# Performance work log

Hardware: AMD Instinct MI355X
Metric: run time of the kernel (lower is better)

## Reference

```python
import jax, jax.numpy as jnp
import numpy as np

B, S, D, HID, NH, R = 64, 2048, 512, 512, 8, 4
DH = D // NH
EPS = 1e-4


def setup_inputs() -> dict:
    key = jax.random.key(0)
    ks = jax.random.split(key, 32)
    w = lambda k, shape: 0.02 * jax.random.normal(k, shape, dtype=jnp.float32)
    embeddings = jax.random.normal(ks[0], (B, S, D), dtype=jnp.float32)
    attention_mask = jax.random.randint(ks[1], (B, S), 0, 2).astype(jnp.int32)
    attention_mask = attention_mask.at[:, 0].set(1)  # guarantee >=1 valid token
    return {
        'embeddings': embeddings,
        'attention_mask': attention_mask,
        # Theory-of-Mind pooled attention
        'Wk': w(ks[2], (D, D)), 'Wv': w(ks[3], (D, D)),
        'q_tom': w(ks[4], (NH, DH)), 'W_tom_fuse': w(ks[5], (D, D)),
        'w_hp': w(ks[6], (D, 1)), 'b_hp': jnp.zeros((1,), jnp.float32),
        # GCACU
        'Wg1': w(ks[7], (D, HID)), 'bg1': jnp.zeros((HID,), jnp.float32),
        'Wg2': w(ks[8], (HID, D)), 'bg2': jnp.zeros((D,), jnp.float32),
        'w_inc': w(ks[9], (D, 1)), 'b_inc': jnp.zeros((1,), jnp.float32),
        # CLoST head (setup/punchline means -> humor prob)
        'Wc1': w(ks[10], (2 * D, HID)), 'bc1': jnp.zeros((HID,), jnp.float32),
        'wc2': w(ks[11], (HID, 1)), 'bc2': jnp.zeros((1,), jnp.float32),
        # mHC low-rank stream mixing
        'U_mhc': w(ks[12], (3, R)), 'V_mhc': w(ks[13], (R, 3)),
        # SEVADE evaluator
        'Ws1': w(ks[14], (D + 3, HID)), 'bs1': jnp.zeros((HID,), jnp.float32),
        'ws2': w(ks[15], (HID, 1)), 'bs2': jnp.zeros((1,), jnp.float32),
        # final head
        'Wf1': w(ks[16], (D + 3, HID)), 'bf1': jnp.zeros((HID,), jnp.float32),
        'wf2': w(ks[17], (HID, 1)), 'bf2': jnp.zeros((1,), jnp.float32),
    }


def safe_logit(p, eps=EPS):
    p = jnp.clip(p, eps, 1.0 - eps)
    return jnp.log(p / (1.0 - p))


def _forward(embeddings, attention_mask, Wk, Wv, q_tom, W_tom_fuse, w_hp, b_hp,
             Wg1, bg1, Wg2, bg2, w_inc, b_inc, Wc1, bc1, wc2, bc2,
             U_mhc, V_mhc, Ws1, bs1, ws2, bs2, Wf1, bf1, wf2, bf2):
    x = embeddings  # [B,S,D]
    m = attention_mask.astype(x.dtype)  # [B,S]

    # --- ToM: learned-query pooled multi-head attention ---
    k = (x @ Wk).reshape(x.shape[0], x.shape[1], NH, DH)  # [B,S,H,dh]
    v = (x @ Wv).reshape(x.shape[0], x.shape[1], NH, DH)
    scores = jnp.einsum('hd,bshd->bhs', q_tom, k) / jnp.sqrt(jnp.float32(DH))
    scores = jnp.where(m[:, None, :] > 0, scores, -1e9)
    attn = jax.nn.softmax(scores, axis=-1)  # [B,H,S]
    fused = jnp.einsum('bhs,bshd->bhd', attn, v).reshape(x.shape[0], D)
    fused_mental = fused @ W_tom_fuse  # [B,D]
    tom_hp = jax.nn.sigmoid(fused_mental @ w_hp + b_hp)  # [B,1]

    # --- GCACU: masked mean -> MLP contextual stream + incongruity ---
    denom = jnp.sum(m, axis=1, keepdims=True)  # [B,1]
    mean_tok = jnp.sum(x * m[..., None], axis=1) / denom  # [B,D]
    ctx = jax.nn.relu(mean_tok @ Wg1 + bg1) @ Wg2 + bg2  # [B,D]
    inc = jax.nn.sigmoid(ctx @ w_inc + b_inc)  # [B,1]

    # --- CLoST: vectorized ragged setup/punchline split (torch code loops per sample) ---
    cum = jnp.cumsum(m, axis=1)  # rank of each valid token, [B,S]
    valid_count = cum[:, -1]  # [B]
    split = jnp.maximum(1, jnp.floor(valid_count * 0.6).astype(jnp.int32)).astype(x.dtype)
    setup_mask = m * (cum <= split[:, None])
    punch_mask = m * (cum > split[:, None])
    punch_cnt = jnp.sum(punch_mask, axis=1, keepdims=True)
    last_mask = m * (cum == valid_count[:, None])  # fallback: last valid token
    punch_mask = jnp.where(punch_cnt > 0, punch_mask, last_mask)
    setup_mean = jnp.sum(x * setup_mask[..., None], 1) / jnp.sum(setup_mask, 1)[:, None]
    punch_mean = jnp.sum(x * punch_mask[..., None], 1) / jnp.sum(punch_mask, 1)[:, None]
    h = jax.nn.relu(jnp.concatenate([setup_mean, punch_mean], -1) @ Wc1 + bc1)
    clost_prob = jax.nn.sigmoid(h @ wc2 + bc2)  # [B,1]
    clost_stream = 0.5 * (setup_mean + punch_mean)  # [B,D]

    scores3 = jnp.concatenate([tom_hp, inc, clost_prob], axis=1)  # [B,3]
    streams = jnp.stack([fused_mental, ctx, clost_stream], axis=1)  # [B,3,D]

    # --- mHC: residual low-rank stream mixing + manifold (unit-norm) constraint ---
    M = jnp.eye(3, dtype=x.dtype) + U_mhc @ V_mhc  # [3,3]
    mixed = jnp.einsum('st,btd->bsd', M, streams)
    mixed = mixed / (jnp.linalg.norm(mixed, axis=-1, keepdims=True) + 1e-6)

    # --- SEVADE evaluator ---
    sev_in = jnp.concatenate([mixed.mean(axis=1), scores3], axis=-1)
    sev_logits = jax.nn.relu(sev_in @ Ws1 + bs1) @ ws2 + bs2  # [B,1]

    # --- final head + logit fusion ---
    pooled = mixed.mean(axis=1)  # [B,D]
    fused_logits = jax.nn.relu(jnp.concatenate([pooled, scores3], -1) @ Wf1 + bf1) @ wf2 + bf2
    logits = fused_logits + 0.5 * sev_logits + 0.1 * safe_logit(scores3.mean(axis=1, keepdims=True))
    return logits  # [B,1]


def reference(embeddings, attention_mask, Wk, Wv, q_tom, W_tom_fuse, w_hp, b_hp,
              Wg1, bg1, Wg2, bg2, w_inc, b_inc, Wc1, bc1, wc2, bc2,
              U_mhc, V_mhc, Ws1, bs1, ws2, bs2, Wf1, bf1, wf2, bf2):
    return _forward(embeddings, attention_mask, Wk, Wv, q_tom, W_tom_fuse, w_hp, b_hp,
                    Wg1, bg1, Wg2, bg2, w_inc, b_inc, Wc1, bc1, wc2, bc2,
                    U_mhc, V_mhc, Ws1, bs1, ws2, bs2, Wf1, bf1, wf2, bf2)
```

## Files before the change

### kernel.cpp

```cpp
#include <hip/hip_runtime.h>
#include <math.h>

#define B_  64
#define S_  2048
#define D_  512
#define NH_ 8

static const size_t OFF_WKEFF  = 0;
static const size_t OFF_SSUM   = 4096;
static const size_t OFF_PSUM   = OFF_SSUM   + 32768;
static const size_t OFF_LSUM   = OFF_PSUM   + 32768;
static const size_t OFF_XAPART = OFF_LSUM   + 512;
static const size_t OFF_XA     = OFF_XAPART + 4194304;
static const size_t OFF_FUSED  = OFF_XA     + 262144;
static const size_t OFF_FM     = OFF_FUSED  + 32768;
static const size_t OFF_MEANT  = OFF_FM     + 32768;
static const size_t OFF_CATSP  = OFF_MEANT  + 32768;
static const size_t OFF_CLOST  = OFF_CATSP  + 65536;
static const size_t OFF_G1     = OFF_CLOST  + 32768;
static const size_t OFF_CTX    = OFF_G1     + 32768;
static const size_t OFF_HC     = OFF_CTX    + 32768;
static const size_t OFF_S3     = OFF_HC     + 32768;
static const size_t OFF_HEADIN = OFF_S3     + 256;
static const size_t OFF_HS     = OFF_HEADIN + 33280;
static const size_t OFF_HF     = OFF_HS     + 32768;
static const size_t OFF_MINFO  = OFF_HF     + 32768;

__global__ __launch_bounds__(256) void k_prep(const float* __restrict__ Wk,
                                              const float* __restrict__ q,
                                              const int* __restrict__ mask,
                                              float* __restrict__ zbase,
                                              float* __restrict__ wkeff,
                                              int* __restrict__ minfo) {
    int bx = blockIdx.x, tid = threadIdx.x;
    if (bx < 258) {
        int i = bx * 256 + tid;
        if (i < 66048) zbase[i] = 0.f;
        return;
    }
    if (bx < 274) {
        int idx = (bx - 258) * 256 + tid;
        int h = idx >> 9, e = idx & 511;
        float s = 0.f;
        #pragma unroll 8
        for (int d = 0; d < 64; ++d) s = fmaf(Wk[e * 512 + h * 64 + d], q[h * 64 + d], s);
        wkeff[h * 512 + e] = s * 0.125f;
        return;
    }
    {
        int b = bx - 274;
        __shared__ int sh[256];
        int m8[8]; int cnt = 0; int s0 = tid * 8;
        #pragma unroll
        for (int i = 0; i < 8; ++i) { m8[i] = mask[b * S_ + s0 + i] > 0; cnt += m8[i]; }
        sh[tid] = cnt; __syncthreads();
        for (int off = 1; off < 256; off <<= 1) {
            int add = (tid >= off) ? sh[tid - off] : 0;
            __syncthreads();
            sh[tid] += add;
            __syncthreads();
        }
        int total  = sh[255];
        int before = sh[tid] - cnt;
        int split  = max(1, (int)floorf((float)total * 0.6f));
        int cum = before;
        #pragma unroll
        for (int i = 0; i < 8; ++i) {
            if (m8[i]) {
                cum++;
                if (cum == split) minfo[b * 8 + 2] = s0 + i;
                if (cum == total) minfo[b * 8 + 3] = s0 + i;
            }
        }
        if (tid == 0) { minfo[b * 8 + 0] = total; minfo[b * 8 + 1] = split; }
    }
}

__global__ __launch_bounds__(256, 4) void k_main(const float* __restrict__ x,
                                                 const int* __restrict__ mask,
                                                 const float* __restrict__ wkeff,
                                                 const int* __restrict__ minfo,
                                                 float* __restrict__ ssum,
                                                 float* __restrict__ psum,
                                                 float* __restrict__ lsum,
                                                 float* __restrict__ xapart) {
    const int b = blockIdx.x, chunk = blockIdx.y;
    const int tid = threadIdx.x, hg = tid >> 6, lane = tid & 63;
    const int h0 = hg * 2;
    const int col0 = lane * 8;

    float wk0[8], wk1[8];
    #pragma unroll
    for (int i = 0; i < 8; ++i) {
        wk0[i] = wkeff[h0 * 512 + col0 + i];
        wk1[i] = wkeff[(h0 + 1) * 512 + col0 + i];
    }

    const int boundary = minfo[b * 8 + 2];
    const float* xb = x + (size_t)b * (S_ * D_);
    const int* mb = mask + b * S_;
    const int sb = chunk * 128;

    int m0 = mb[sb + lane];
    int m1 = mb[sb + 64 + lane];

    float xacc0[8], xacc1[8], sacc[8], pacc[8];
    #pragma unroll
    for (int i = 0; i < 8; ++i) { xacc0[i] = 0.f; xacc1[i] = 0.f; sacc[i] = 0.f; pacc[i] = 0.f; }
    float lacc0 = 0.f, lacc1 = 0.f;

    const float* base = xb + (size_t)sb * D_ + col0;
    float4 A0 = *(const float4*)(base);
    float4 A1 = *(const float4*)(base + 4);
    float4 B0 = *(const float4*)(base + D_);
    float4 B1 = *(const float4*)(base + D_ + 4);

    for (int t = 0; t < 128; t += 2) {
        float xa8[8] = {A0.x, A0.y, A0.z, A0.w, A1.x, A1.y, A1.z, A1.w};
        float xb8[8] = {B0.x, B0.y, B0.z, B0.w, B1.x, B1.y, B1.z, B1.w};
        if (t + 2 < 128) {
            const float* nb = base + (size_t)(t + 2) * D_;
            A0 = *(const float4*)(nb);
            A1 = *(const float4*)(nb + 4);
            B0 = *(const float4*)(nb + D_);
            B1 = *(const float4*)(nb + D_ + 4);
        }
        float s00 = xa8[0] * wk0[0], s01 = xa8[0] * wk1[0];
        float s10 = xb8[0] * wk0[0], s11 = xb8[0] * wk1[0];
        #pragma unroll
        for (int i = 1; i < 8; ++i) {
            s00 = fmaf(xa8[i], wk0[i], s00);
            s01 = fmaf(xa8[i], wk1[i], s01);
            s10 = fmaf(xb8[i], wk0[i], s10);
            s11 = fmaf(xb8[i], wk1[i], s11);
        }
        #pragma unroll
        for (int d = 1; d < 64; d <<= 1) {
            s00 += __shfl_xor(s00, d, 64);
            s01 += __shfl_xor(s01, d, 64);
            s10 += __shfl_xor(s10, d, 64);
            s11 += __shfl_xor(s11, d, 64);
        }
        int mreg = (t & 64) ? m1 : m0;
        int mm0 = __shfl(mreg, t & 63, 64);
        int mm1 = __shfl(mreg, (t + 1) & 63, 64);
        int sg0 = sb + t, sg1 = sb + t + 1;

        float w00 = (mm0 > 0) ? __expf(s00) : 0.f;
        float w01 = (mm0 > 0) ? __expf(s01) : 0.f;
        float w10 = (mm1 > 0) ? __expf(s10) : 0.f;
        float w11 = (mm1 > 0) ? __expf(s11) : 0.f;
        lacc0 += w00 + w10;
        lacc1 += w01 + w11;
        #pragma unroll
        for (int i = 0; i < 8; ++i) {
            xacc0[i] = fmaf(w10, xb8[i], fmaf(w00, xa8[i], xacc0[i]));
            xacc1[i] = fmaf(w11, xb8[i], fmaf(w01, xa8[i], xacc1[i]));
        }
        if (hg == 0) {
            float fs0 = (mm0 > 0 && sg0 <= boundary) ? 1.f : 0.f;
            float fp0 = (mm0 > 0 && sg0 >  boundary) ? 1.f : 0.f;
            float fs1 = (mm1 > 0 && sg1 <= boundary) ? 1.f : 0.f;
            float fp1 = (mm1 > 0 && sg1 >  boundary) ? 1.f : 0.f;
            #pragma unroll
            for (int i = 0; i < 8; ++i) {
                sacc[i] = fmaf(fs1, xb8[i], fmaf(fs0, xa8[i], sacc[i]));
                pacc[i] = fmaf(fp1, xb8[i], fmaf(fp0, xa8[i], pacc[i]));
            }
        }
    }

    float* d0 = xapart + (((size_t)b * 16 + chunk) * 8 + h0) * 512 + col0;
    float* d1 = d0 + 512;
    ((float4*)d0)[0] = make_float4(xacc0[0], xacc0[1], xacc0[2], xacc0[3]);
    ((float4*)d0)[1] = make_float4(xacc0[4], xacc0[5], xacc0[6], xacc0[7]);
    ((float4*)d1)[0] = make_float4(xacc1[0], xacc1[1], xacc1[2], xacc1[3]);
    ((float4*)d1)[1] = make_float4(xacc1[4], xacc1[5], xacc1[6], xacc1[7]);
    if (lane == 0) {
        atomicAdd(&lsum[b * 8 + h0],     lacc0);
        atomicAdd(&lsum[b * 8 + h0 + 1], lacc1);
    }
    if (hg == 0) {
        #pragma unroll
        for (int i = 0; i < 8; ++i) {
            atomicAdd(&ssum[b * 512 + col0 + i], sacc[i]);
            atomicAdd(&psum[b * 512 + col0 + i], pacc[i]);
        }
    }
}

__global__ __launch_bounds__(256) void k_xared(const float* __restrict__ part,
                                               const float* __restrict__ lsum,
                                               float* __restrict__ xa) {
    int idx = blockIdx.x * 256 + threadIdx.x;
    int b = idx >> 12, j = idx & 4095, h = j >> 9;
    float s = 0.f;
    #pragma unroll
    for (int c = 0; c < 16; ++c) s += part[((size_t)(b * 16 + c)) * 4096 + j];
    xa[idx] = s / lsum[b * 8 + h];
}

__global__ __launch_bounds__(256) void k_means(const float* __restrict__ x,
                                               const float* __restrict__ ssum,
                                               const float* __restrict__ psum,
                                               const int* __restrict__ minfo,
                                               float* __restrict__ meantok,
                                               float* __restrict__ catsp,
                                               float* __restrict__ clost) {
    int b = blockIdx.x;
    int e = blockIdx.y * 256 + threadIdx.x;
    int total = minfo[b * 8 + 0], split = minfo[b * 8 + 1], last = minfo[b * 8 + 3];
    int pcnt = total - split;
    float ssv = ssum[b * 512 + e], psv = psum[b * 512 + e];
    float mt = (ssv + psv) / (float)total;
    float sm = ssv / (float)split;
    float pm = (pcnt > 0) ? psv / (float)pcnt : x[((size_t)b * S_ + last) * D_ + e];
    meantok[b * 512 + e] = mt;
    catsp[b * 1024 + e] = sm;
    catsp[b * 1024 + 512 + e] = pm;
    clost[b * 512 + e] = 0.5f * (sm + pm);
}

__global__ __launch_bounds__(256) void k_gemv3(
    const float* A0_, int lda0, const float* W0_, const float* bi0_, float* o0_, int K0, int r0, int hm0,
    const float* A1_, int lda1, const float* W1_, const float* bi1_, float* o1_, int K1, int r1, int hm1,
    const float* A2_, int lda2, const float* W2_, const float* bi2_, float* o2_, int K2, int r2, int hm2) {
    const float* A; const float* W; const float* bias; float* out;
    int lda, K, relu_, hm;
    int z = blockIdx.z;
    if (z == 0)      { A = A0_; lda = lda0; W = W0_; bias = bi0_; out = o0_; K = K0; relu_ = r0; hm = hm0; }
    else if (z == 1) { A = A1_; lda = lda1; W = W1_; bias = bi1_; out = o1_; K = K1; relu_ = r1; hm = hm1; }
    else             { A = A2_; lda = lda2; W = W2_; bias = bi2_; out = o2_; K = K2; relu_ = r2; hm = hm2; }

    int b = blockIdx.x, jg = blockIdx.y;
    int tid = threadIdx.x, jl = tid & 63, part = tid >> 6;
    int j = jg * 64 + jl;
    const float* a = hm ? (A + ((size_t)(b * 8 + jg)) * 512) : (A + (size_t)b * lda);

    __shared__ float sha[1024];
    for (int e = tid; e < K; e += 256) sha[e] = a[e];
    __syncthreads();

    int Kq = (K + 3) >> 2;
    int e0 = part * Kq, e1 = min(K, e0 + Kq);
    float acc = 0.f;
    int e = e0;
    for (; e + 8 <= e1; e += 8) {
        #pragma unroll
        for (int u = 0; u < 8; ++u)
            acc = fmaf(sha[e + u], W[(size_t)(e + u) * 512 + j], acc);
    }
    for (; e < e1; ++e) acc = fmaf(sha[e], W[(size_t)e * 512 + j], acc);

    __shared__ float shr[256];
    shr[tid] = acc;
    __syncthreads();
    if (part == 0) {
        float s = shr[jl] + shr[jl + 64] + shr[jl + 128] + shr[jl + 192];
        if (bias) s += bias[j];
        if (relu_) s = fmaxf(s, 0.f);
        out[(size_t)b * 512 + j] = s;
    }
}

__global__ __launch_bounds__(256) void k_scalmix(const float* __restrict__ fm,
                                                 const float* __restrict__ ctx,
                                                 const float* __restrict__ hc,
                                                 const float* __restrict__ clost,
                                                 const float* __restrict__ w_hp,  const float* __restrict__ b_hp,
                                                 const float* __restrict__ w_inc, const float* __restrict__ b_inc,
                                                 const float* __restrict__ wc2,   const float* __restrict__ bc2,
                                                 const float* __restrict__ U,
                                                 const float* __restrict__ V,
                                                 float* __restrict__ s3,
                                                 float* __restrict__ headin) {
    int b = blockIdx.x, tid = threadIdx.x;
    float a0 = 0.f, a1 = 0.f, a2 = 0.f;
    for (int e = tid; e < 512; e += 256) {
        a0 = fmaf(fm[b * 512 + e],  w_hp[e],  a0);
        a1 = fmaf(ctx[b * 512 + e], w_inc[e], a1);
        a2 = fmaf(hc[b * 512 + e],  wc2[e],   a2);
    }
    __shared__ float r[3][256];
    r[0][tid] = a0; r[1][tid] = a1; r[2][tid] = a2;
    __syncthreads();
    for (int off = 128; off > 0; off >>= 1) {
        if (tid < off) {
            r[0][tid] += r[0][tid + off];
            r[1][tid] += r[1][tid + off];
            r[2][tid] += r[2][tid + off];
        }
        __syncthreads();
    }
    __shared__ float s3sh[3];
    if (tid == 0) {
        s3sh[0] = 1.f / (1.f + __expf(-(r[0][0] + b_hp[0])));
        s3sh[1] = 1.f / (1.f + __expf(-(r[1][0] + b_inc[0])));
        s3sh[2] = 1.f / (1.f + __expf(-(r[2][0] + bc2[0])));
        s3[b * 4 + 0] = s3sh[0];
        s3[b * 4 + 1] = s3sh[1];
        s3[b * 4 + 2] = s3sh[2];
    }
    __syncthreads();
    float M3[3][3];
    #pragma unroll
    for (int s = 0; s < 3; ++s)
        #pragma unroll
        for (int t = 0; t < 3; ++t) {
            float acc = (s == t) ? 1.f : 0.f;
            #pragma unroll
            for (int r4 = 0; r4 < 4; ++r4) acc = fmaf(U[s * 4 + r4], V[r4 * 3 + t], acc);
            M3[s][t] = acc;
        }
    float mx[3][2];
    #pragma unroll
    for (int kk = 0; kk < 2; ++kk) {
        int e = tid + kk * 256;
        float t0 = fm[b * 512 + e], t1 = ctx[b * 512 + e], t2 = clost[b * 512 + e];
        #pragma unroll
        for (int s = 0; s < 3; ++s) mx[s][kk] = M3[s][0] * t0 + M3[s][1] * t1 + M3[s][2] * t2;
    }
    #pragma unroll
    for (int s = 0; s < 3; ++s) r[s][tid] = mx[s][0] * mx[s][0] + mx[s][1] * mx[s][1];
    __syncthreads();
    for (int off = 128; off > 0; off >>= 1) {
        if (tid < off) {
            r[0][tid] += r[0][tid + off];
            r[1][tid] += r[1][tid + off];
            r[2][tid] += r[2][tid + off];
        }
        __syncthreads();
    }
    __shared__ float nrm[3];
    if (tid < 3) nrm[tid] = sqrtf(r[tid][0]) + 1e-6f;
    __syncthreads();
    #pragma unroll
    for (int kk = 0; kk < 2; ++kk) {
        int e = tid + kk * 256;
        float p = (mx[0][kk] / nrm[0] + mx[1][kk] / nrm[1] + mx[2][kk] / nrm[2]) * (1.f / 3.f);
        headin[b * 520 + e] = p;
    }
    if (tid < 3) headin[b * 520 + 512 + tid] = s3sh[tid];
}

__global__ __launch_bounds__(256) void k_logit(const float* __restrict__ hs,
                                               const float* __restrict__ hf,
                                               const float* __restrict__ ws2, const float* __restrict__ bs2,
                                               const float* __restrict__ wf2, const float* __restrict__ bf2,
                                               const float* __restrict__ s3,
                                               float* __restrict__ out) {
    int b = blockIdx.x, tid = threadIdx.x;
    float a = 0.f, c = 0.f;
    for (int e = tid; e < 512; e += 256) {
        a = fmaf(hs[b * 512 + e], ws2[e], a);
        c = fmaf(hf[b * 512 + e], wf2[e], c);
    }
    __shared__ float r[2][256];
    r[0][tid] = a; r[1][tid] = c;
    __syncthreads();
    for (int off = 128; off > 0; off >>= 1) {
        if (tid < off) { r[0][tid] += r[0][tid + off]; r[1][tid] += r[1][tid + off]; }
        __syncthreads();
    }
    if (tid == 0) {
        float sev = r[0][0] + bs2[0];
        float fl  = r[1][0] + bf2[0];
        float p = (s3[b * 4] + s3[b * 4 + 1] + s3[b * 4 + 2]) * (1.f / 3.f);
        p = fminf(fmaxf(p, 1e-4f), 1.f - 1e-4f);
        out[b] = fl + 0.5f * sev + 0.1f * logf(p / (1.f - p));
    }
}

extern "C" void kernel_launch(void* const* d_in, const int* in_sizes, int n_in,
                              void* d_out, int out_size, void* d_ws, size_t ws_size,
                              hipStream_t stream) {
    const float* x     = (const float*)d_in[0];
    const int*   mask  = (const int*)d_in[1];
    const float* Wk    = (const float*)d_in[2];
    const float* Wv    = (const float*)d_in[3];
    const float* q_tom = (const float*)d_in[4];
    const float* Wtf   = (const float*)d_in[5];
    const float* w_hp  = (const float*)d_in[6];
    const float* b_hp  = (const float*)d_in[7];
    const float* Wg1   = (const float*)d_in[8];
    const float* bg1   = (const float*)d_in[9];
    const float* Wg2   = (const float*)d_in[10];
    const float* bg2   = (const float*)d_in[11];
    const float* w_inc = (const float*)d_in[12];
    const float* b_inc = (const float*)d_in[13];
    const float* Wc1   = (const float*)d_in[14];
    const float* bc1   = (const float*)d_in[15];
    const float* wc2   = (const float*)d_in[16];
    const float* bc2   = (const float*)d_in[17];
    const float* U     = (const float*)d_in[18];
    const float* V     = (const float*)d_in[19];
    const float* Ws1   = (const float*)d_in[20];
    const float* bs1   = (const float*)d_in[21];
    const float* ws2   = (const float*)d_in[22];
    const float* bs2   = (const float*)d_in[23];
    const float* Wf1   = (const float*)d_in[24];
    const float* bf1   = (const float*)d_in[25];
    const float* wf2   = (const float*)d_in[26];
    const float* bf2   = (const float*)d_in[27];

    float* ws      = (float*)d_ws;
    float* wkeff   = ws + OFF_WKEFF;
    float* ssum    = ws + OFF_SSUM;
    float* psum    = ws + OFF_PSUM;
    float* lsum    = ws + OFF_LSUM;
    float* xapart  = ws + OFF_XAPART;
    float* xa      = ws + OFF_XA;
    float* fused   = ws + OFF_FUSED;
    float* fm      = ws + OFF_FM;
    float* meantok = ws + OFF_MEANT;
    float* catsp   = ws + OFF_CATSP;
    float* clost   = ws + OFF_CLOST;
    float* g1      = ws + OFF_G1;
    float* ctxb    = ws + OFF_CTX;
    float* hc      = ws + OFF_HC;
    float* s3      = ws + OFF_S3;
    float* headin  = ws + OFF_HEADIN;
    float* hsb     = ws + OFF_HS;
    float* hfb     = ws + OFF_HF;
    int*   minfo   = (int*)(ws + OFF_MINFO);
    float* out     = (float*)d_out;

    hipLaunchKernelGGL(k_prep,   dim3(338),      dim3(256), 0, stream, Wk, q_tom, mask, ssum, wkeff, minfo);
    hipLaunchKernelGGL(k_main,   dim3(64, 16),   dim3(256), 0, stream, x, mask, wkeff, minfo,
                       ssum, psum, lsum, xapart);
    hipLaunchKernelGGL(k_xared,  dim3(1024),     dim3(256), 0, stream, xapart, lsum, xa);
    hipLaunchKernelGGL(k_means,  dim3(64, 2),    dim3(256), 0, stream, x, ssum, psum, minfo,
                       meantok, catsp, clost);
    hipLaunchKernelGGL(k_gemv3,  dim3(64, 8, 3), dim3(256), 0, stream,
                       xa, 0, Wv, (const float*)nullptr, fused, 512, 0, 1,
                       meantok, 512, Wg1, bg1, g1, 512, 1, 0,
                       catsp, 1024, Wc1, bc1, hc, 1024, 1, 0);
    hipLaunchKernelGGL(k_gemv3,  dim3(64, 8, 2), dim3(256), 0, stream,
                       fused, 512, Wtf, (const float*)nullptr, fm, 512, 0, 0,
                       g1, 512, Wg2, bg2, ctxb, 512, 0, 0,
                       (const float*)nullptr, 0, (const float*)nullptr, (const float*)nullptr,
                       (float*)nullptr, 0, 0, 0);
    hipLaunchKernelGGL(k_scalmix, dim3(64),      dim3(256), 0, stream, fm, ctxb, hc, clost,
                       w_hp, b_hp, w_inc, b_inc, wc2, bc2, U, V, s3, headin);
    hipLaunchKernelGGL(k_gemv3,  dim3(64, 8, 2), dim3(256), 0, stream,
                       headin, 520, Ws1, bs1, hsb, 515, 1, 0,
                       headin, 520, Wf1, bf1, hfb, 515, 1, 0,
                       (const float*)nullptr, 0, (const float*)nullptr, (const float*)nullptr,
                       (float*)nullptr, 0, 0, 0);
    hipLaunchKernelGGL(k_logit,  dim3(64),       dim3(256), 0, stream, hsb, hfb, ws2, bs2, wf2, bf2, s3, out);
}
```

Measured before the change: 510.9 us.

## Accumulate attention-pooled x via atomics, drop partial-sum reduction kernel, unroll 4 tokens

The main kernel now adds its per-chunk weighted sums straight into a zeroed per-batch/head buffer with atomics, rather than writing 16 partials that a separate kernel reduced. The softmax normalisation by lsum moves into the gemv's shared-memory load, which removes the k_xared launch and its 16 MB partial buffer traffic. The inner loop handles 4 tokens per iteration with 4-row prefetch and mask bits taken from a ballot. Occupancy is lowered to 3 blocks per CU so the extra registers fit. The costs are more float atomics (16 chunks contend per address), a larger zeroing pass in k_prep, and nondeterministic summation order.

```diff
diff --git a/kernel.cpp b/kernel.cpp
--- a/kernel.cpp
+++ b/kernel.cpp
@@ -8,23 +8,24 @@
 
 static const size_t OFF_WKEFF  = 0;
 static const size_t OFF_SSUM   = 4096;
-static const size_t OFF_PSUM   = OFF_SSUM   + 32768;
-static const size_t OFF_LSUM   = OFF_PSUM   + 32768;
-static const size_t OFF_XAPART = OFF_LSUM   + 512;
-static const size_t OFF_XA     = OFF_XAPART + 4194304;
-static const size_t OFF_FUSED  = OFF_XA     + 262144;
-static const size_t OFF_FM     = OFF_FUSED  + 32768;
-static const size_t OFF_MEANT  = OFF_FM     + 32768;
-static const size_t OFF_CATSP  = OFF_MEANT  + 32768;
-static const size_t OFF_CLOST  = OFF_CATSP  + 65536;
-static const size_t OFF_G1     = OFF_CLOST  + 32768;
-static const size_t OFF_CTX    = OFF_G1     + 32768;
-static const size_t OFF_HC     = OFF_CTX    + 32768;
-static const size_t OFF_S3     = OFF_HC     + 32768;
-static const size_t OFF_HEADIN = OFF_S3     + 256;
-static const size_t OFF_HS     = OFF_HEADIN + 33280;
-static const size_t OFF_HF     = OFF_HS     + 32768;
-static const size_t OFF_MINFO  = OFF_HF     + 32768;
+static const size_t OFF_PSUM   = 36864;
+static const size_t OFF_LSUM   = 69632;
+static const size_t OFF_XARAW  = 70144;
+static const size_t OFF_FUSED  = 332288;
+static const size_t OFF_FM     = 365056;
+static const size_t OFF_MEANT  = 397824;
+static const size_t OFF_CATSP  = 430592;
+static const size_t OFF_CLOST  = 496128;
+static const size_t OFF_G1     = 528896;
+static const size_t OFF_CTX    = 561664;
+static const size_t OFF_HC     = 594432;
+static const size_t OFF_S3     = 627200;
+static const size_t OFF_HEADIN = 627456;
+static const size_t OFF_HS     = 660736;
+static const size_t OFF_HF     = 693504;
+static const size_t OFF_MINFO  = 726272;
+
+#define NZERO 328192
 
 __global__ __launch_bounds__(256) void k_prep(const float* __restrict__ Wk,
                                               const float* __restrict__ q,
@@ -33,13 +34,13 @@
                                               float* __restrict__ wkeff,
                                               int* __restrict__ minfo) {
     int bx = blockIdx.x, tid = threadIdx.x;
-    if (bx < 258) {
+    if (bx < 1282) {
         int i = bx * 256 + tid;
-        if (i < 66048) zbase[i] = 0.f;
+        if (i < NZERO) zbase[i] = 0.f;
         return;
     }
-    if (bx < 274) {
-        int idx = (bx - 258) * 256 + tid;
+    if (bx < 1298) {
+        int idx = (bx - 1282) * 256 + tid;
         int h = idx >> 9, e = idx & 511;
         float s = 0.f;
         #pragma unroll 8
@@ -48,7 +49,7 @@
         return;
     }
     {
-        int b = bx - 274;
+        int b = bx - 1298;
         __shared__ int sh[256];
         int m8[8]; int cnt = 0; int s0 = tid * 8;
         #pragma unroll
@@ -76,14 +77,14 @@
     }
 }
 
-__global__ __launch_bounds__(256, 4) void k_main(const float* __restrict__ x,
+__global__ __launch_bounds__(256, 3) void k_main(const float* __restrict__ x,
                                                  const int* __restrict__ mask,
                                                  const float* __restrict__ wkeff,
                                                  const int* __restrict__ minfo,
                                                  float* __restrict__ ssum,
                                                  float* __restrict__ psum,
                                                  float* __restrict__ lsum,
-                                                 float* __restrict__ xapart) {
+                                                 float* __restrict__ xaraw) {
     const int b = blockIdx.x, chunk = blockIdx.y;
     const int tid = threadIdx.x, hg = tid >> 6, lane = tid & 63;
     const int h0 = hg * 2;
@@ -97,88 +98,111 @@
     }
 
     const int boundary = minfo[b * 8 + 2];
-    const float* xb = x + (size_t)b * (S_ * D_);
+    const int sb = chunk * 128;
     const int* mb = mask + b * S_;
-    const int sb = chunk * 128;
-
-    int m0 = mb[sb + lane];
-    int m1 = mb[sb + 64 + lane];
-
-    float xacc0[8], xacc1[8], sacc[8], pacc[8];
-    #pragma unroll
-    for (int i = 0; i < 8; ++i) { xacc0[i] = 0.f; xacc1[i] = 0.f; sacc[i] = 0.f; pacc[i] = 0.f; }
-    float lacc0 = 0.f, lacc1 = 0.f;
-
-    const float* base = xb + (size_t)sb * D_ + col0;
-    float4 A0 = *(const float4*)(base);
-    float4 A1 = *(const float4*)(base + 4);
-    float4 B0 = *(const float4*)(base + D_);
-    float4 B1 = *(const float4*)(base + D_ + 4);
-
-    for (int t = 0; t < 128; t += 2) {
-        float xa8[8] = {A0.x, A0.y, A0.z, A0.w, A1.x, A1.y, A1.z, A1.w};
-        float xb8[8] = {B0.x, B0.y, B0.z, B0.w, B1.x, B1.y, B1.z, B1.w};
-        if (t + 2 < 128) {
-            const float* nb = base + (size_t)(t + 2) * D_;
-            A0 = *(const float4*)(nb);
-            A1 = *(const float4*)(nb + 4);
-            B0 = *(const float4*)(nb + D_);
-            B1 = *(const float4*)(nb + D_ + 4);
-        }
-        float s00 = xa8[0] * wk0[0], s01 = xa8[0] * wk1[0];
-        float s10 = xb8[0] * wk0[0], s11 = xb8[0] * wk1[0];
-        #pragma unroll
-        for (int i = 1; i < 8; ++i) {
-            s00 = fmaf(xa8[i], wk0[i], s00);
-            s01 = fmaf(xa8[i], wk1[i], s01);
-            s10 = fmaf(xb8[i], wk0[i], s10);
-            s11 = fmaf(xb8[i], wk1[i], s11);
+    unsigned long long bm0 = __ballot(mb[sb + lane] > 0);
+    unsigned long long bm1 = __ballot(mb[sb + 64 + lane] > 0);
+
+    float acc0[8], acc1[8], sacc[8], pacc[8];
+    #pragma unroll
+    for (int i = 0; i < 8; ++i) { acc0[i] = 0.f; acc1[i] = 0.f; sacc[i] = 0.f; pacc[i] = 0.f; }
+    float l0 = 0.f, l1 = 0.f;
+
+    const float* base = x + (size_t)b * (S_ * D_) + (size_t)sb * D_ + col0;
+
+    float4 P[8];
+    #pragma unroll
+    for (int k = 0; k < 4; ++k) {
+        P[2 * k]     = *(const float4*)(base + (size_t)k * D_);
+        P[2 * k + 1] = *(const float4*)(base + (size_t)k * D_ + 4);
+    }
+
+    for (int t = 0; t < 128; t += 4) {
+        float cur[4][8];
+        #pragma unroll
+        for (int k = 0; k < 4; ++k) {
+            cur[k][0] = P[2 * k].x;     cur[k][1] = P[2 * k].y;
+            cur[k][2] = P[2 * k].z;     cur[k][3] = P[2 * k].w;
+            cur[k][4] = P[2 * k + 1].x; cur[k][5] = P[2 * k + 1].y;
+            cur[k][6] = P[2 * k + 1].z; cur[k][7] = P[2 * k + 1].w;
+        }
+        if (t + 4 < 128) {
+            const float* nb = base + (size_t)(t + 4) * D_;
+            #pragma unroll
+            for (int k = 0; k < 4; ++k) {
+                P[2 * k]     = *(const float4*)(nb + (size_t)k * D_);
+                P[2 * k + 1] = *(const float4*)(nb + (size_t)k * D_ + 4);
+            }
+        }
+        float s8[8];
+        #pragma unroll
+        for (int k = 0; k < 4; ++k) {
+            float a0 = cur[k][0] * wk0[0];
+            float a1 = cur[k][0] * wk1[0];
+            #pragma unroll
+            for (int i = 1; i < 8; ++i) {
+                a0 = fmaf(cur[k][i], wk0[i], a0);
+                a1 = fmaf(cur[k][i], wk1[i], a1);
+            }
+            s8[k] = a0; s8[4 + k] = a1;
         }
         #pragma unroll
         for (int d = 1; d < 64; d <<= 1) {
-            s00 += __shfl_xor(s00, d, 64);
-            s01 += __shfl_xor(s01, d, 64);
-            s10 += __shfl_xor(s10, d, 64);
-            s11 += __shfl_xor(s11, d, 64);
-        }
-        int mreg = (t & 64) ? m1 : m0;
-        int mm0 = __shfl(mreg, t & 63, 64);
-        int mm1 = __shfl(mreg, (t + 1) & 63, 64);
-        int sg0 = sb + t, sg1 = sb + t + 1;
-
-        float w00 = (mm0 > 0) ? __expf(s00) : 0.f;
-        float w01 = (mm0 > 0) ? __expf(s01) : 0.f;
-        float w10 = (mm1 > 0) ? __expf(s10) : 0.f;
-        float w11 = (mm1 > 0) ? __expf(s11) : 0.f;
-        lacc0 += w00 + w10;
-        lacc1 += w01 + w11;
+            #pragma unroll
+            for (int v = 0; v < 8; ++v) s8[v] += __shfl_xor(s8[v], d, 64);
+        }
+        unsigned long long bsel = (t < 64) ? bm0 : bm1;
+        float w0[4], w1[4];
+        #pragma unroll
+        for (int k = 0; k < 4; ++k) {
+            bool mm = ((bsel >> ((t + k) & 63)) & 1ULL) != 0;
+            w0[k] = mm ? __expf(s8[k])     : 0.f;
+            w1[k] = mm ? __expf(s8[4 + k]) : 0.f;
+        }
+        l0 += (w0[0] + w0[1]) + (w0[2] + w0[3]);
+        l1 += (w1[0] + w1[1]) + (w1[2] + w1[3]);
         #pragma unroll
         for (int i = 0; i < 8; ++i) {
-            xacc0[i] = fmaf(w10, xb8[i], fmaf(w00, xa8[i], xacc0[i]));
-            xacc1[i] = fmaf(w11, xb8[i], fmaf(w01, xa8[i], xacc1[i]));
+            float a = acc0[i], c = acc1[i];
+            #pragma unroll
+            for (int k = 0; k < 4; ++k) {
+                a = fmaf(w0[k], cur[k][i], a);
+                c = fmaf(w1[k], cur[k][i], c);
+            }
+            acc0[i] = a; acc1[i] = c;
         }
         if (hg == 0) {
-            float fs0 = (mm0 > 0 && sg0 <= boundary) ? 1.f : 0.f;
-            float fp0 = (mm0 > 0 && sg0 >  boundary) ? 1.f : 0.f;
-            float fs1 = (mm1 > 0 && sg1 <= boundary) ? 1.f : 0.f;
-            float fp1 = (mm1 > 0 && sg1 >  boundary) ? 1.f : 0.f;
+            float fs[4], fp[4];
+            #pragma unroll
+            for (int k = 0; k < 4; ++k) {
+                bool mm = ((bsel >> ((t + k) & 63)) & 1ULL) != 0;
+                int sg = sb + t + k;
+                fs[k] = (mm && sg <= boundary) ? 1.f : 0.f;
+                fp[k] = (mm && sg >  boundary) ? 1.f : 0.f;
+            }
             #pragma unroll
             for (int i = 0; i < 8; ++i) {
-                sacc[i] = fmaf(fs1, xb8[i], fmaf(fs0, xa8[i], sacc[i]));
-                pacc[i] = fmaf(fp1, xb8[i], fmaf(fp0, xa8[i], pacc[i]));
-            }
-        }
-    }
-
-    float* d0 = xapart + (((size_t)b * 16 + chunk) * 8 + h0) * 512 + col0;
-    float* d1 = d0 + 512;
-    ((float4*)d0)[0] = make_float4(xacc0[0], xacc0[1], xacc0[2], xacc0[3]);
-    ((float4*)d0)[1] = make_float4(xacc0[4], xacc0[5], xacc0[6], xacc0[7]);
-    ((float4*)d1)[0] = make_float4(xacc1[0], xacc1[1], xacc1[2], xacc1[3]);
-    ((float4*)d1)[1] = make_float4(xacc1[4], xacc1[5], xacc1[6], xacc1[7]);
+                float a = sacc[i], c = pacc[i];
+                #pragma unroll
+                for (int k = 0; k < 4; ++k) {
+                    a = fmaf(fs[k], cur[k][i], a);
+                    c = fmaf(fp[k], cur[k][i], c);
+                }
+                sacc[i] = a; pacc[i] = c;
+            }
+        }
+    }
+
+    float* xr0 = xaraw + ((size_t)(b * 8 + h0)) * 512 + col0;
+    float* xr1 = xr0 + 512;
+    #pragma unroll
+    for (int i = 0; i < 8; ++i) {
+        atomicAdd(&xr0[i], acc0[i]);
+        atomicAdd(&xr1[i], acc1[i]);
+    }
     if (lane == 0) {
-        atomicAdd(&lsum[b * 8 + h0],     lacc0);
-        atomicAdd(&lsum[b * 8 + h0 + 1], lacc1);
+        atomicAdd(&lsum[b * 8 + h0],     l0);
+        atomicAdd(&lsum[b * 8 + h0 + 1], l1);
     }
     if (hg == 0) {
         #pragma unroll
@@ -187,17 +211,6 @@
             atomicAdd(&psum[b * 512 + col0 + i], pacc[i]);
         }
     }
-}
-
-__global__ __launch_bounds__(256) void k_xared(const float* __restrict__ part,
-                                               const float* __restrict__ lsum,
-                                               float* __restrict__ xa) {
-    int idx = blockIdx.x * 256 + threadIdx.x;
-    int b = idx >> 12, j = idx & 4095, h = j >> 9;
-    float s = 0.f;
-    #pragma unroll
-    for (int c = 0; c < 16; ++c) s += part[((size_t)(b * 16 + c)) * 4096 + j];
-    xa[idx] = s / lsum[b * 8 + h];
 }
 
 __global__ __launch_bounds__(256) void k_means(const float* __restrict__ x,
@@ -222,6 +235,7 @@
 }
 
 __global__ __launch_bounds__(256) void k_gemv3(
+    const float* lsum,
     const float* A0_, int lda0, const float* W0_, const float* bi0_, float* o0_, int K0, int r0, int hm0,
     const float* A1_, int lda1, const float* W1_, const float* bi1_, float* o1_, int K1, int r1, int hm1,
     const float* A2_, int lda2, const float* W2_, const float* bi2_, float* o2_, int K2, int r2, int hm2) {
@@ -236,9 +250,10 @@
     int tid = threadIdx.x, jl = tid & 63, part = tid >> 6;
     int j = jg * 64 + jl;
     const float* a = hm ? (A + ((size_t)(b * 8 + jg)) * 512) : (A + (size_t)b * lda);
+    float scale = hm ? (1.f / lsum[b * 8 + jg]) : 1.f;
 
     __shared__ float sha[1024];
-    for (int e = tid; e < K; e += 256) sha[e] = a[e];
+    for (int e = tid; e < K; e += 256) sha[e] = a[e] * scale;
     __syncthreads();
 
     int Kq = (K + 3) >> 2;
@@ -408,8 +423,7 @@
     float* ssum    = ws + OFF_SSUM;
     float* psum    = ws + OFF_PSUM;
     float* lsum    = ws + OFF_LSUM;
-    float* xapart  = ws + OFF_XAPART;
-    float* xa      = ws + OFF_XA;
+    float* xaraw   = ws + OFF_XARAW;
     float* fused   = ws + OFF_FUSED;
     float* fm      = ws + OFF_FM;
     float* meantok = ws + OFF_MEANT;
@@ -425,24 +439,23 @@
     int*   minfo   = (int*)(ws + OFF_MINFO);
     float* out     = (float*)d_out;
 
-    hipLaunchKernelGGL(k_prep,   dim3(338),      dim3(256), 0, stream, Wk, q_tom, mask, ssum, wkeff, minfo);
+    hipLaunchKernelGGL(k_prep,   dim3(1362),     dim3(256), 0, stream, Wk, q_tom, mask, ssum, wkeff, minfo);
     hipLaunchKernelGGL(k_main,   dim3(64, 16),   dim3(256), 0, stream, x, mask, wkeff, minfo,
-                       ssum, psum, lsum, xapart);
-    hipLaunchKernelGGL(k_xared,  dim3(1024),     dim3(256), 0, stream, xapart, lsum, xa);
+                       ssum, psum, lsum, xaraw);
     hipLaunchKernelGGL(k_means,  dim3(64, 2),    dim3(256), 0, stream, x, ssum, psum, minfo,
                        meantok, catsp, clost);
-    hipLaunchKernelGGL(k_gemv3,  dim3(64, 8, 3), dim3(256), 0, stream,
-                       xa, 0, Wv, (const float*)nullptr, fused, 512, 0, 1,
+    hipLaunchKernelGGL(k_gemv3,  dim3(64, 8, 3), dim3(256), 0, stream, lsum,
+                       xaraw, 0, Wv, (const float*)nullptr, fused, 512, 0, 1,
                        meantok, 512, Wg1, bg1, g1, 512, 1, 0,
                        catsp, 1024, Wc1, bc1, hc, 1024, 1, 0);
-    hipLaunchKernelGGL(k_gemv3,  dim3(64, 8, 2), dim3(256), 0, stream,
+    hipLaunchKernelGGL(k_gemv3,  dim3(64, 8, 2), dim3(256), 0, stream, lsum,
                        fused, 512, Wtf, (const float*)nullptr, fm, 512, 0, 0,
                        g1, 512, Wg2, bg2, ctxb, 512, 0, 0,
                        (const float*)nullptr, 0, (const float*)nullptr, (const float*)nullptr,
                        (float*)nullptr, 0, 0, 0);
     hipLaunchKernelGGL(k_scalmix, dim3(64),      dim3(256), 0, stream, fm, ctxb, hc, clost,
                        w_hp, b_hp, w_inc, b_inc, wc2, bc2, U, V, s3, headin);
-    hipLaunchKernelGGL(k_gemv3,  dim3(64, 8, 2), dim3(256), 0, stream,
+    hipLaunchKernelGGL(k_gemv3,  dim3(64, 8, 2), dim3(256), 0, stream, lsum,
                        headin, 520, Ws1, bs1, hsb, 515, 1, 0,
                        headin, 520, Wf1, bf1, hfb, 515, 1, 0,
                        (const float*)nullptr, 0, (const float*)nullptr, (const float*)nullptr,
```

Result: slower. 621.7 us (+21.7%).

## Replace atomics with partial buffers, DPP wave reductions, and ballot masks

Applied to the files above, without the earlier changes.

The main streaming kernel now writes per-chunk partial sums for the setup/punchline means and the softmax denominators, instead of issuing global atomicAdds. The reduction kernel sums all ten rows, and the softmax normalisation moves into the GEMV input load. The zeroing pass in the prep kernel goes away. The per-token 64-lane shuffle reductions become DPP row/bcast steps plus a readlane, and the mask is held as ballot bitmasks rather than fetched by shuffles. This trades atomic contention and shuffle latency for a somewhat larger partial buffer and an extra reduction read.

```diff
diff --git a/kernel.cpp b/kernel.cpp
--- a/kernel.cpp
+++ b/kernel.cpp
@@ -7,39 +7,46 @@
 #define NH_ 8
 
 static const size_t OFF_WKEFF  = 0;
-static const size_t OFF_SSUM   = 4096;
-static const size_t OFF_PSUM   = OFF_SSUM   + 32768;
-static const size_t OFF_LSUM   = OFF_PSUM   + 32768;
-static const size_t OFF_XAPART = OFF_LSUM   + 512;
-static const size_t OFF_XA     = OFF_XAPART + 4194304;
-static const size_t OFF_FUSED  = OFF_XA     + 262144;
-static const size_t OFF_FM     = OFF_FUSED  + 32768;
-static const size_t OFF_MEANT  = OFF_FM     + 32768;
-static const size_t OFF_CATSP  = OFF_MEANT  + 32768;
-static const size_t OFF_CLOST  = OFF_CATSP  + 65536;
-static const size_t OFF_G1     = OFF_CLOST  + 32768;
-static const size_t OFF_CTX    = OFF_G1     + 32768;
-static const size_t OFF_HC     = OFF_CTX    + 32768;
-static const size_t OFF_S3     = OFF_HC     + 32768;
-static const size_t OFF_HEADIN = OFF_S3     + 256;
-static const size_t OFF_HS     = OFF_HEADIN + 33280;
-static const size_t OFF_HF     = OFF_HS     + 32768;
-static const size_t OFF_MINFO  = OFF_HF     + 32768;
+static const size_t OFF_XPART  = 4096;
+static const size_t OFF_LPART  = 5246976;
+static const size_t OFF_XA     = 5255168;
+static const size_t OFF_SSUM   = 5517312;
+static const size_t OFF_PSUM   = 5550080;
+static const size_t OFF_FUSED  = 5582848;
+static const size_t OFF_FM     = 5615616;
+static const size_t OFF_MEANT  = 5648384;
+static const size_t OFF_CATSP  = 5681152;
+static const size_t OFF_CLOST  = 5746688;
+static const size_t OFF_G1     = 5779456;
+static const size_t OFF_CTX    = 5812224;
+static const size_t OFF_HC     = 5844992;
+static const size_t OFF_S3     = 5877760;
+static const size_t OFF_HEADIN = 5878016;
+static const size_t OFF_HS     = 5911296;
+static const size_t OFF_HF     = 5944064;
+static const size_t OFF_MINFO  = 5976832;
+
+__device__ __forceinline__ float wave_sum64(float v) {
+#define DPP_STEP(ctrl, rm) \
+    v += __int_as_float(__builtin_amdgcn_update_dpp(0, __float_as_int(v), (ctrl), (rm), 0xf, true))
+    DPP_STEP(0x111, 0xf);
+    DPP_STEP(0x112, 0xf);
+    DPP_STEP(0x114, 0xf);
+    DPP_STEP(0x118, 0xf);
+    DPP_STEP(0x142, 0xa);
+    DPP_STEP(0x143, 0xc);
+#undef DPP_STEP
+    return __int_as_float(__builtin_amdgcn_readlane(__float_as_int(v), 63));
+}
 
 __global__ __launch_bounds__(256) void k_prep(const float* __restrict__ Wk,
                                               const float* __restrict__ q,
                                               const int* __restrict__ mask,
-                                              float* __restrict__ zbase,
                                               float* __restrict__ wkeff,
                                               int* __restrict__ minfo) {
     int bx = blockIdx.x, tid = threadIdx.x;
-    if (bx < 258) {
-        int i = bx * 256 + tid;
-        if (i < 66048) zbase[i] = 0.f;
-        return;
-    }
-    if (bx < 274) {
-        int idx = (bx - 258) * 256 + tid;
+    if (bx < 16) {
+        int idx = bx * 256 + tid;
         int h = idx >> 9, e = idx & 511;
         float s = 0.f;
         #pragma unroll 8
@@ -48,7 +55,7 @@
         return;
     }
     {
-        int b = bx - 274;
+        int b = bx - 16;
         __shared__ int sh[256];
         int m8[8]; int cnt = 0; int s0 = tid * 8;
         #pragma unroll
@@ -80,10 +87,8 @@
                                                  const int* __restrict__ mask,
                                                  const float* __restrict__ wkeff,
                                                  const int* __restrict__ minfo,
-                                                 float* __restrict__ ssum,
-                                                 float* __restrict__ psum,
-                                                 float* __restrict__ lsum,
-                                                 float* __restrict__ xapart) {
+                                                 float* __restrict__ xpart,
+                                                 float* __restrict__ lpart) {
     const int b = blockIdx.x, chunk = blockIdx.y;
     const int tid = threadIdx.x, hg = tid >> 6, lane = tid & 63;
     const int h0 = hg * 2;
@@ -97,19 +102,17 @@
     }
 
     const int boundary = minfo[b * 8 + 2];
-    const float* xb = x + (size_t)b * (S_ * D_);
+    const int sb = chunk * 128;
     const int* mb = mask + b * S_;
-    const int sb = chunk * 128;
-
-    int m0 = mb[sb + lane];
-    int m1 = mb[sb + 64 + lane];
-
-    float xacc0[8], xacc1[8], sacc[8], pacc[8];
-    #pragma unroll
-    for (int i = 0; i < 8; ++i) { xacc0[i] = 0.f; xacc1[i] = 0.f; sacc[i] = 0.f; pacc[i] = 0.f; }
-    float lacc0 = 0.f, lacc1 = 0.f;
-
-    const float* base = xb + (size_t)sb * D_ + col0;
+    unsigned long long bm0 = __ballot(mb[sb + lane] > 0);
+    unsigned long long bm1 = __ballot(mb[sb + 64 + lane] > 0);
+
+    float acc0[8], acc1[8], sacc[8], pacc[8];
+    #pragma unroll
+    for (int i = 0; i < 8; ++i) { acc0[i] = 0.f; acc1[i] = 0.f; sacc[i] = 0.f; pacc[i] = 0.f; }
+    float l0 = 0.f, l1 = 0.f;
+
+    const float* base = x + (size_t)b * (S_ * D_) + (size_t)sb * D_ + col0;
     float4 A0 = *(const float4*)(base);
     float4 A1 = *(const float4*)(base + 4);
     float4 B0 = *(const float4*)(base + D_);
@@ -134,34 +137,32 @@
             s10 = fmaf(xb8[i], wk0[i], s10);
             s11 = fmaf(xb8[i], wk1[i], s11);
         }
-        #pragma unroll
-        for (int d = 1; d < 64; d <<= 1) {
-            s00 += __shfl_xor(s00, d, 64);
-            s01 += __shfl_xor(s01, d, 64);
-            s10 += __shfl_xor(s10, d, 64);
-            s11 += __shfl_xor(s11, d, 64);
-        }
-        int mreg = (t & 64) ? m1 : m0;
-        int mm0 = __shfl(mreg, t & 63, 64);
-        int mm1 = __shfl(mreg, (t + 1) & 63, 64);
-        int sg0 = sb + t, sg1 = sb + t + 1;
-
-        float w00 = (mm0 > 0) ? __expf(s00) : 0.f;
-        float w01 = (mm0 > 0) ? __expf(s01) : 0.f;
-        float w10 = (mm1 > 0) ? __expf(s10) : 0.f;
-        float w11 = (mm1 > 0) ? __expf(s11) : 0.f;
-        lacc0 += w00 + w10;
-        lacc1 += w01 + w11;
+        float f00 = wave_sum64(s00);
+        float f01 = wave_sum64(s01);
+        float f10 = wave_sum64(s10);
+        float f11 = wave_sum64(s11);
+
+        unsigned long long bsel = (t < 64) ? bm0 : bm1;
+        bool mm0 = ((bsel >> (t & 63)) & 1ULL) != 0;
+        bool mm1 = ((bsel >> ((t + 1) & 63)) & 1ULL) != 0;
+
+        float w00 = mm0 ? __expf(f00) : 0.f;
+        float w01 = mm0 ? __expf(f01) : 0.f;
+        float w10 = mm1 ? __expf(f10) : 0.f;
+        float w11 = mm1 ? __expf(f11) : 0.f;
+        l0 += w00 + w10;
+        l1 += w01 + w11;
         #pragma unroll
         for (int i = 0; i < 8; ++i) {
-            xacc0[i] = fmaf(w10, xb8[i], fmaf(w00, xa8[i], xacc0[i]));
-            xacc1[i] = fmaf(w11, xb8[i], fmaf(w01, xa8[i], xacc1[i]));
+            acc0[i] = fmaf(w10, xb8[i], fmaf(w00, xa8[i], acc0[i]));
+            acc1[i] = fmaf(w11, xb8[i], fmaf(w01, xa8[i], acc1[i]));
         }
         if (hg == 0) {
-            float fs0 = (mm0 > 0 && sg0 <= boundary) ? 1.f : 0.f;
-            float fp0 = (mm0 > 0 && sg0 >  boundary) ? 1.f : 0.f;
-            float fs1 = (mm1 > 0 && sg1 <= boundary) ? 1.f : 0.f;
-            float fp1 = (mm1 > 0 && sg1 >  boundary) ? 1.f : 0.f;
+            int sg0 = sb + t, sg1 = sb + t + 1;
+            float fs0 = (mm0 && sg0 <= boundary) ? 1.f : 0.f;
+            float fp0 = (mm0 && sg0 >  boundary) ? 1.f : 0.f;
+            float fs1 = (mm1 && sg1 <= boundary) ? 1.f : 0.f;
+            float fp1 = (mm1 && sg1 >  boundary) ? 1.f : 0.f;
             #pragma unroll
             for (int i = 0; i < 8; ++i) {
                 sacc[i] = fmaf(fs1, xb8[i], fmaf(fs0, xa8[i], sacc[i]));
@@ -170,34 +171,40 @@
         }
     }
 
-    float* d0 = xapart + (((size_t)b * 16 + chunk) * 8 + h0) * 512 + col0;
+    float* pbase = xpart + ((size_t)(b * 16 + chunk) * 10) * 512;
+    float* d0 = pbase + (size_t)h0 * 512 + col0;
     float* d1 = d0 + 512;
-    ((float4*)d0)[0] = make_float4(xacc0[0], xacc0[1], xacc0[2], xacc0[3]);
-    ((float4*)d0)[1] = make_float4(xacc0[4], xacc0[5], xacc0[6], xacc0[7]);
-    ((float4*)d1)[0] = make_float4(xacc1[0], xacc1[1], xacc1[2], xacc1[3]);
-    ((float4*)d1)[1] = make_float4(xacc1[4], xacc1[5], xacc1[6], xacc1[7]);
+    ((float4*)d0)[0] = make_float4(acc0[0], acc0[1], acc0[2], acc0[3]);
+    ((float4*)d0)[1] = make_float4(acc0[4], acc0[5], acc0[6], acc0[7]);
+    ((float4*)d1)[0] = make_float4(acc1[0], acc1[1], acc1[2], acc1[3]);
+    ((float4*)d1)[1] = make_float4(acc1[4], acc1[5], acc1[6], acc1[7]);
+    if (hg == 0) {
+        float* ds = pbase + 8 * 512 + col0;
+        float* dp = pbase + 9 * 512 + col0;
+        ((float4*)ds)[0] = make_float4(sacc[0], sacc[1], sacc[2], sacc[3]);
+        ((float4*)ds)[1] = make_float4(sacc[4], sacc[5], sacc[6], sacc[7]);
+        ((float4*)dp)[0] = make_float4(pacc[0], pacc[1], pacc[2], pacc[3]);
+        ((float4*)dp)[1] = make_float4(pacc[4], pacc[5], pacc[6], pacc[7]);
+    }
     if (lane == 0) {
-        atomicAdd(&lsum[b * 8 + h0],     lacc0);
-        atomicAdd(&lsum[b * 8 + h0 + 1], lacc1);
-    }
-    if (hg == 0) {
-        #pragma unroll
-        for (int i = 0; i < 8; ++i) {
-            atomicAdd(&ssum[b * 512 + col0 + i], sacc[i]);
-            atomicAdd(&psum[b * 512 + col0 + i], pacc[i]);
-        }
+        lpart[(b * 16 + chunk) * 8 + h0]     = l0;
+        lpart[(b * 16 + chunk) * 8 + h0 + 1] = l1;
     }
 }
 
 __global__ __launch_bounds__(256) void k_xared(const float* __restrict__ part,
-                                               const float* __restrict__ lsum,
-                                               float* __restrict__ xa) {
-    int idx = blockIdx.x * 256 + threadIdx.x;
-    int b = idx >> 12, j = idx & 4095, h = j >> 9;
+                                               float* __restrict__ xa,
+                                               float* __restrict__ ssum,
+                                               float* __restrict__ psum) {
+    int b = blockIdx.x, r = blockIdx.y;
+    int e = blockIdx.z * 256 + threadIdx.x;
     float s = 0.f;
     #pragma unroll
-    for (int c = 0; c < 16; ++c) s += part[((size_t)(b * 16 + c)) * 4096 + j];
-    xa[idx] = s / lsum[b * 8 + h];
+    for (int c = 0; c < 16; ++c)
+        s += part[(((size_t)(b * 16 + c)) * 10 + r) * 512 + e];
+    if (r < 8)       xa[((size_t)b * 8 + r) * 512 + e] = s;
+    else if (r == 8) ssum[b * 512 + e] = s;
+    else             psum[b * 512 + e] = s;
 }
 
 __global__ __launch_bounds__(256) void k_means(const float* __restrict__ x,
@@ -222,6 +229,7 @@
 }
 
 __global__ __launch_bounds__(256) void k_gemv3(
+    const float* lpart,
     const float* A0_, int lda0, const float* W0_, const float* bi0_, float* o0_, int K0, int r0, int hm0,
     const float* A1_, int lda1, const float* W1_, const float* bi1_, float* o1_, int K1, int r1, int hm1,
     const float* A2_, int lda2, const float* W2_, const float* bi2_, float* o2_, int K2, int r2, int hm2) {
@@ -236,9 +244,16 @@
     int tid = threadIdx.x, jl = tid & 63, part = tid >> 6;
     int j = jg * 64 + jl;
     const float* a = hm ? (A + ((size_t)(b * 8 + jg)) * 512) : (A + (size_t)b * lda);
+    float scale = 1.f;
+    if (hm) {
+        float lsum = 0.f;
+        #pragma unroll
+        for (int c = 0; c < 16; ++c) lsum += lpart[(b * 16 + c) * 8 + jg];
+        scale = 1.f / lsum;
+    }
 
     __shared__ float sha[1024];
-    for (int e = tid; e < K; e += 256) sha[e] = a[e];
+    for (int e = tid; e < K; e += 256) sha[e] = a[e] * scale;
     __syncthreads();
 
     int Kq = (K + 3) >> 2;
@@ -405,11 +420,11 @@
 
     float* ws      = (float*)d_ws;
     float* wkeff   = ws + OFF_WKEFF;
+    float* xpart   = ws + OFF_XPART;
+    float* lpart   = ws + OFF_LPART;
+    float* xa      = ws + OFF_XA;
     float* ssum    = ws + OFF_SSUM;
     float* psum    = ws + OFF_PSUM;
-    float* lsum    = ws + OFF_LSUM;
-    float* xapart  = ws + OFF_XAPART;
-    float* xa      = ws + OFF_XA;
     float* fused   = ws + OFF_FUSED;
     float* fm      = ws + OFF_FM;
     float* meantok = ws + OFF_MEANT;
@@ -425,27 +440,27 @@
     int*   minfo   = (int*)(ws + OFF_MINFO);
     float* out     = (float*)d_out;
 
-    hipLaunchKernelGGL(k_prep,   dim3(338),      dim3(256), 0, stream, Wk, q_tom, mask, ssum, wkeff, minfo);
-    hipLaunchKernelGGL(k_main,   dim3(64, 16),   dim3(256), 0, stream, x, mask, wkeff, minfo,
-                       ssum, psum, lsum, xapart);
-    hipLaunchKernelGGL(k_xared,  dim3(1024),     dim3(256), 0, stream, xapart, lsum, xa);
-    hipLaunchKernelGGL(k_means,  dim3(64, 2),    dim3(256), 0, stream, x, ssum, psum, minfo,
+    hipLaunchKernelGGL(k_prep,   dim3(80),        dim3(256), 0, stream, Wk, q_tom, mask, wkeff, minfo);
+    hipLaunchKernelGGL(k_main,   dim3(64, 16),    dim3(256), 0, stream, x, mask, wkeff, minfo,
+                       xpart, lpart);
+    hipLaunchKernelGGL(k_xared,  dim3(64, 10, 2), dim3(256), 0, stream, xpart, xa, ssum, psum);
+    hipLaunchKernelGGL(k_means,  dim3(64, 2),     dim3(256), 0, stream, x, ssum, psum, minfo,
                        meantok, catsp, clost);
-    hipLaunchKernelGGL(k_gemv3,  dim3(64, 8, 3), dim3(256), 0, stream,
+    hipLaunchKernelGGL(k_gemv3,  dim3(64, 8, 3),  dim3(256), 0, stream, lpart,
                        xa, 0, Wv, (const float*)nullptr, fused, 512, 0, 1,
                        meantok, 512, Wg1, bg1, g1, 512, 1, 0,
                        catsp, 1024, Wc1, bc1, hc, 1024, 1, 0);
-    hipLaunchKernelGGL(k_gemv3,  dim3(64, 8, 2), dim3(256), 0, stream,
+    hipLaunchKernelGGL(k_gemv3,  dim3(64, 8, 2),  dim3(256), 0, stream, lpart,
                        fused, 512, Wtf, (const float*)nullptr, fm, 512, 0, 0,
                        g1, 512, Wg2, bg2, ctxb, 512, 0, 0,
                        (const float*)nullptr, 0, (const float*)nullptr, (const float*)nullptr,
                        (float*)nullptr, 0, 0, 0);
-    hipLaunchKernelGGL(k_scalmix, dim3(64),      dim3(256), 0, stream, fm, ctxb, hc, clost,
+    hipLaunchKernelGGL(k_scalmix, dim3(64),       dim3(256), 0, stream, fm, ctxb, hc, clost,
                        w_hp, b_hp, w_inc, b_inc, wc2, bc2, U, V, s3, headin);
-    hipLaunchKernelGGL(k_gemv3,  dim3(64, 8, 2), dim3(256), 0, stream,
+    hipLaunchKernelGGL(k_gemv3,  dim3(64, 8, 2),  dim3(256), 0, stream, lpart,
                        headin, 520, Ws1, bs1, hsb, 515, 1, 0,
                        headin, 520, Wf1, bf1, hfb, 515, 1, 0,
                        (const float*)nullptr, 0, (const float*)nullptr, (const float*)nullptr,
                        (float*)nullptr, 0, 0, 0);
-    hipLaunchKernelGGL(k_logit,  dim3(64),       dim3(256), 0, stream, hsb, hfb, ws2, bs2, wf2, bf2, s3, out);
-}
+    hipLaunchKernelGGL(k_logit,  dim3(64),        dim3(256), 0, stream, hsb, hfb, ws2, bs2, wf2, bf2, s3, out);
+}
```

Result: faster. 494.2 us (-3.3%).
